# Performance work log

Measured on AMD Instinct MI355X. Metric: run time of the kernel, lower is better.

## Reference

```python
import jax, jax.numpy as jnp
import numpy as np


def setup_inputs() -> dict:
    key = jax.random.key(0)
    ks = jax.random.split(key, 8)
    B, C, H, W = 4, 256, 64, 64
    Cqk = C // 8
    s = 0.05
    return {
        "x": jax.random.normal(ks[0], (B, C, H, W), jnp.float32),
        "Wq": jax.random.normal(ks[1], (Cqk, C), jnp.float32) * s,
        "bq": jax.random.normal(ks[2], (Cqk,), jnp.float32) * s,
        "Wk": jax.random.normal(ks[3], (Cqk, C), jnp.float32) * s,
        "bk": jax.random.normal(ks[4], (Cqk,), jnp.float32) * s,
        "Wv": jax.random.normal(ks[5], (C, C), jnp.float32) * s,
        "bv": jax.random.normal(ks[6], (C,), jnp.float32) * s,
        "gamma": jax.random.normal(ks[7], (1,), jnp.float32),
    }


def reference(x, Wq, bq, Wk, bk, Wv, bv, gamma):
    B, C, H, W = x.shape
    N = H * W
    xf = x.reshape(B, C, N)                      # [B,C,N]
    # 1x1 convs == channel matmuls
    q = jnp.einsum('oc,bcn->bon', Wq, xf) + bq[None, :, None]   # [B,C/8,N]
    k = jnp.einsum('oc,bcn->bon', Wk, xf) + bk[None, :, None]   # [B,C/8,N]
    v = jnp.einsum('oc,bcn->bon', Wv, xf) + bv[None, :, None]   # [B,C,N]
    # scores[b,i,j] = <q[:,i], k[:,j]>; softmax over j (last dim)
    scores = jnp.einsum('bci,bcj->bij', q, k)                   # [B,N,N]
    attn = jax.nn.softmax(scores, axis=-1)
    # out[b,c,i] = sum_j v[b,c,j] * attn[b,i,j]
    out = jnp.einsum('bcj,bij->bci', v, attn).reshape(B, C, H, W)
    return gamma[0] * out + x
```

## Files before the change

kernel.cpp:

```cpp
#include <hip/hip_runtime.h>


#define B_ 4
#define C_ 256
#define N_ 4096
#define CQK 32

typedef __attribute__((ext_vector_type(8))) short short8;
typedef __attribute__((ext_vector_type(4))) short short4v;
typedef __attribute__((ext_vector_type(16))) float f32x16;
typedef __attribute__((ext_vector_type(4))) float f32x4;

__device__ __forceinline__ unsigned short f2bf(float f) {
  unsigned int u = __builtin_bit_cast(unsigned int, f);
  u = (u + 0x7fffu + ((u >> 16) & 1u)) >> 16;
  return (unsigned short)u;
}
__device__ __forceinline__ float bf2f(unsigned short s) {
  unsigned int u = ((unsigned int)s) << 16;
  return __builtin_bit_cast(float, u);
}
__device__ __forceinline__ short f32tof16(float f) {
  const _Float16 hf = (_Float16)f;
  return __builtin_bit_cast(short, hf);
}
__device__ __forceinline__ f32x16 mfma16(short8 a, short8 b, f32x16 c) {
  return __builtin_amdgcn_mfma_f32_32x32x16_bf16(a, b, c, 0, 0, 0);
}
__device__ __forceinline__ int swz64(int row, int col) {
  return row * 64 + ((((col >> 3) ^ row) & 7) << 3) + (col & 7);
}

#define WAITCNT(s) asm volatile("s_waitcnt " s ::: "memory")
#define BARRIER()                         \
  do {                                    \
    __builtin_amdgcn_s_barrier();         \
    asm volatile("" ::: "memory");        \
  } while (0)

__global__ __launch_bounds__(256) void k_prep(
    const float* __restrict__ x, unsigned short* __restrict__ xthi,
    unsigned short* __restrict__ xtlo,
    const float* __restrict__ Wq, const float* __restrict__ Wk,
    const float* __restrict__ Wv,
    unsigned short* __restrict__ wqh, unsigned short* __restrict__ wql,
    unsigned short* __restrict__ wkh, unsigned short* __restrict__ wkl,
    unsigned short* __restrict__ wvh, unsigned short* __restrict__ wvl) {
  __shared__ __align__(16) float tile[64 * 65];
  const int bi = blockIdx.x;
  const int t = threadIdx.x;
  if (bi < 1024) {
    const int it = bi & 63, ct = (bi >> 6) & 3, b = bi >> 8;
    const int i0 = it * 64, c0 = ct * 64;
    {
      const int i = t & 63, cb = t >> 6;
#pragma unroll
      for (int z = 0; z < 16; ++z) {
        const int c = z * 4 + cb;
        tile[i * 65 + c] = x[(b * C_ + c0 + c) * N_ + i0 + i];
      }
    }
    __syncthreads();
    {
      const int ii = t >> 2, p = t & 3;
      short8 h0, h1, l0, l1;
#pragma unroll
      for (int e = 0; e < 16; ++e) {
        const float f = tile[ii * 65 + p * 16 + e];
        const unsigned short hb = f2bf(f);
        const unsigned short lb = f2bf(f - bf2f(hb));
        if (e < 8) { h0[e] = (short)hb; l0[e] = (short)lb; }
        else       { h1[e - 8] = (short)hb; l1[e - 8] = (short)lb; }
      }
      const int base = (b * N_ + i0 + ii) * C_ + c0 + p * 16;
      *(short8*)(xthi + base) = h0;
      *(short8*)(xthi + base + 8) = h1;
      *(short8*)(xtlo + base) = l0;
      *(short8*)(xtlo + base + 8) = l1;
    }
  } else {
    const int e = (bi - 1024) * 256 + t;
    const float* src; unsigned short *hi, *lo; int idx;
    if (e < 8192)        { src = Wq; hi = wqh; lo = wql; idx = e; }
    else if (e < 16384)  { src = Wk; hi = wkh; lo = wkl; idx = e - 8192; }
    else                 { src = Wv; hi = wvh; lo = wvl; idx = e - 16384; }
    const float f = src[idx];
    const unsigned short h = f2bf(f);
    hi[idx] = h;
    lo[idx] = f2bf(f - bf2f(h));
  }
}

__global__ __launch_bounds__(256) void k_proj(
    const unsigned short* __restrict__ wqh, const unsigned short* __restrict__ wql,
    const unsigned short* __restrict__ wkh, const unsigned short* __restrict__ wkl,
    const unsigned short* __restrict__ wvh, const unsigned short* __restrict__ wvl,
    const unsigned short* __restrict__ xthi, const unsigned short* __restrict__ xtlo,
    const float* __restrict__ bq, const float* __restrict__ bk,
    const float* __restrict__ bv,
    unsigned short* __restrict__ qhg, unsigned short* __restrict__ qlg,
    unsigned short* __restrict__ khg, unsigned short* __restrict__ klg,
    unsigned short* __restrict__ vg) {
  __shared__ __align__(16) char sm[33792];
  unsigned short* awh = (unsigned short*)sm;
  unsigned short* awl = awh + 4096;
  unsigned short* bxh = awl + 4096;
  unsigned short* bxl = bxh + 4096;
  float* qt = (float*)sm;

  const int it = blockIdx.x, ot = blockIdx.y, b = blockIdx.z;
  const int i0 = it * 64, o0 = ot * 64;
  const int t = threadIdx.x, lane = t & 63, w = t >> 6, h = lane >> 5;
  const int mb = w >> 1, nb = w & 1;
  const int srow = t >> 2, sp = t & 3;

  const int og = o0 + srow;
  const unsigned short *wh, *wl;
  if (og < 32)      { wh = wqh + og * C_;        wl = wql + og * C_; }
  else if (og < 64) { wh = wkh + (og - 32) * C_; wl = wkl + (og - 32) * C_; }
  else              { wh = wvh + (og - 64) * C_; wl = wvl + (og - 64) * C_; }
  const unsigned short* xh = xthi + (b * N_ + i0 + srow) * C_;
  const unsigned short* xl = xtlo + (b * N_ + i0 + srow) * C_;

  f32x16 acc;
#pragma unroll
  for (int e = 0; e < 16; ++e) acc[e] = 0.f;
  const int m = 32 * mb + (lane & 31);
  const int n = 32 * nb + (lane & 31);

  for (int kt = 0; kt < 4; ++kt) {
    const int cb = kt * 64 + sp * 16;
    *(short8*)&awh[swz64(srow, sp * 16)]     = *(const short8*)(wh + cb);
    *(short8*)&awh[swz64(srow, sp * 16 + 8)] = *(const short8*)(wh + cb + 8);
    *(short8*)&awl[swz64(srow, sp * 16)]     = *(const short8*)(wl + cb);
    *(short8*)&awl[swz64(srow, sp * 16 + 8)] = *(const short8*)(wl + cb + 8);
    *(short8*)&bxh[swz64(srow, sp * 16)]     = *(const short8*)(xh + cb);
    *(short8*)&bxh[swz64(srow, sp * 16 + 8)] = *(const short8*)(xh + cb + 8);
    *(short8*)&bxl[swz64(srow, sp * 16)]     = *(const short8*)(xl + cb);
    *(short8*)&bxl[swz64(srow, sp * 16 + 8)] = *(const short8*)(xl + cb + 8);
    __syncthreads();
#pragma unroll
    for (int kk = 0; kk < 4; ++kk) {
      const int kb = kk * 16 + h * 8;
      const short8 ah  = *(const short8*)&awh[swz64(m, kb)];
      const short8 al2 = *(const short8*)&awl[swz64(m, kb)];
      const short8 bh  = *(const short8*)&bxh[swz64(n, kb)];
      const short8 bl2 = *(const short8*)&bxl[swz64(n, kb)];
      acc = mfma16(ah, bh, acc);
      acc = mfma16(ah, bl2, acc);
      acc = mfma16(al2, bh, acc);
    }
    __syncthreads();
  }

  if (ot > 0) {
#pragma unroll
    for (int e = 0; e < 16; ++e) {
      const int r = 32 * mb + (e & 3) + 8 * (e >> 2) + 4 * h;
      const int oc = o0 - 64 + r;
      vg[(b * C_ + oc) * N_ + i0 + n] = f2bf(acc[e] + bv[oc]);
    }
  } else {
#pragma unroll
    for (int e = 0; e < 16; ++e) {
      const int r = 32 * mb + (e & 3) + 8 * (e >> 2) + 4 * h;
      const float bias = (r < 32) ? bq[r] : bk[r - 32];
      qt[r * 65 + n] = acc[e] + bias;
    }
    __syncthreads();
    const int ii = t >> 2;
    short8 hv0, hv1, lv0, lv1;
#pragma unroll
    for (int e = 0; e < 16; ++e) {
      const float f = qt[(sp * 16 + e) * 65 + ii];
      const unsigned short hb = f2bf(f);
      const unsigned short lb = f2bf(f - bf2f(hb));
      if (e < 8) { hv0[e] = (short)hb; lv0[e] = (short)lb; }
      else       { hv1[e - 8] = (short)hb; lv1[e - 8] = (short)lb; }
    }
    if (sp < 2) {
      const int base = (b * N_ + i0 + ii) * CQK + sp * 16;
      *(short8*)(qhg + base) = hv0; *(short8*)(qhg + base + 8) = hv1;
      *(short8*)(qlg + base) = lv0; *(short8*)(qlg + base + 8) = lv1;
    } else {
      const int base = (b * N_ + i0 + ii) * CQK + sp * 16 - 32;
      *(short8*)(khg + base) = hv0; *(short8*)(khg + base + 8) = hv1;
      *(short8*)(klg + base) = lv0; *(short8*)(klg + base + 8) = lv1;
    }
  }
}

__global__ __launch_bounds__(768, 3) void k_flash(
    const unsigned short* __restrict__ qhg, const unsigned short* __restrict__ qlg,
    const unsigned short* __restrict__ khg, const unsigned short* __restrict__ klg,
    const unsigned short* __restrict__ vg,
    unsigned short* __restrict__ Opart, float* __restrict__ mlpart) {
  __shared__ __align__(16) char sm[17920];
  char* Pb0 = sm;
  char* Pb1 = sm + 8192;
  float* alphaA = (float*)(sm + 16384);
  float* mlm = (float*)(sm + 16896);

  const int blk = blockIdx.x;
  const int b = (blk >> 1) & 3;
  const int half = blk & 1;
  const int qt_ = blk >> 3;
  const int q0 = qt_ * 64;
  const int jbase = half * 2048;
  const int t = threadIdx.x, lane = t & 63, w = t >> 6, h = lane >> 5;
  const int l31 = lane & 31;

  if (w < 8) {
    const int c = 32 * w + l31;
    const unsigned short* vsrc = vg + (size_t)(b * C_ + c) * N_ + jbase + h * 8;
    f32x16 acc0, acc1;
#pragma unroll
    for (int e = 0; e < 16; ++e) { acc0[e] = 0.f; acc1[e] = 0.f; }
    short8 vf[4];
#pragma unroll
    for (int kk = 0; kk < 4; ++kk)
      vf[kk] = *(const short8*)(vsrc + kk * 16);
    WAITCNT("lgkmcnt(0)");
    BARRIER();

#pragma unroll 2
    for (int kt = 0; kt < 32; ++kt) {
      const char* pb = (kt & 1) ? Pb1 : Pb0;
      const float* alp = alphaA + (kt & 1) * 64;
#pragma unroll
      for (int eq = 0; eq < 4; ++eq) {
        const f32x4 av0 = *(const f32x4*)(alp + 8 * eq + 4 * h);
        const f32x4 av1 = *(const f32x4*)(alp + 32 + 8 * eq + 4 * h);
#pragma unroll
        for (int q = 0; q < 4; ++q) {
          acc0[4 * eq + q] *= av0[q];
          acc1[4 * eq + q] *= av1[q];
        }
      }
      __builtin_amdgcn_s_setprio(1);
#pragma unroll
      for (int kk = 0; kk < 4; ++kk) {
        const int phys = (2 * kk + h) ^ (l31 & 7);
        const short8 pa0 = *(const short8*)(pb + l31 * 128 + phys * 16);
        const short8 pa1 = *(const short8*)(pb + (32 + l31) * 128 + phys * 16);
        acc0 = mfma16(pa0, vf[kk], acc0);
        acc1 = mfma16(pa1, vf[kk], acc1);
      }
      __builtin_amdgcn_s_setprio(0);
      if (kt + 1 < 32) {
#pragma unroll
        for (int kk = 0; kk < 4; ++kk)
          vf[kk] = *(const short8*)(vsrc + (kt + 1) * 64 + kk * 16);
      }
      WAITCNT("lgkmcnt(0)");
      BARRIER();
    }
    {
      unsigned short* dst = Opart + (size_t)blk * 16384 + (w * 64 + lane) * 32;
      short8 o0, o1, o2, o3;
#pragma unroll
      for (int e = 0; e < 8; ++e) {
        o0[e] = f32tof16(acc0[e]);
        o1[e] = f32tof16(acc0[8 + e]);
        o2[e] = f32tof16(acc1[e]);
        o3[e] = f32tof16(acc1[8 + e]);
      }
      *(short8*)(dst) = o0;
      *(short8*)(dst + 8) = o1;
      *(short8*)(dst + 16) = o2;
      *(short8*)(dst + 24) = o3;
    }
  } else {
    const int sw = w - 8;
    const int pair = sw >> 1;
    const int rb = sw & 1;
    const int srow = rb * 32 + l31;
    short8 qfh[2], qfl[2];
    {
      const unsigned short* qph = qhg + (size_t)(b * N_ + q0 + srow) * CQK + h * 8;
      const unsigned short* qpl = qlg + (size_t)(b * N_ + q0 + srow) * CQK + h * 8;
#pragma unroll
      for (int kk = 0; kk < 2; ++kk) {
        qfh[kk] = *(const short8*)(qph + kk * 16);
        qfl[kk] = *(const short8*)(qpl + kk * 16);
      }
    }
    const unsigned short* kph = khg + (size_t)(b * N_ + jbase + l31) * CQK + h * 8;
    const unsigned short* kpl = klg + (size_t)(b * N_ + jbase + l31) * CQK + h * 8;
    short8 kfh[2][2], kfl[2][2];
    float m_run = -1e30f, l_run = 0.f;

    auto loadK = [&](int tau) {
#pragma unroll
      for (int jt = 0; jt < 2; ++jt)
#pragma unroll
        for (int kk = 0; kk < 2; ++kk) {
          kfh[jt][kk] = *(const short8*)(kph + tau * 2048 + jt * 1024 + kk * 16);
          kfl[jt][kk] = *(const short8*)(kpl + tau * 2048 + jt * 1024 + kk * 16);
        }
    };
    auto s_step = [&](int tau) {
      f32x16 s0, s1;
#pragma unroll
      for (int e = 0; e < 16; ++e) { s0[e] = 0.f; s1[e] = 0.f; }
      __builtin_amdgcn_s_setprio(1);
#pragma unroll
      for (int kk = 0; kk < 2; ++kk) {
        s0 = mfma16(kfh[0][kk], qfh[kk], s0);
        s0 = mfma16(kfh[0][kk], qfl[kk], s0);
        s0 = mfma16(kfl[0][kk], qfh[kk], s0);
        s1 = mfma16(kfh[1][kk], qfh[kk], s1);
        s1 = mfma16(kfh[1][kk], qfl[kk], s1);
        s1 = mfma16(kfl[1][kk], qfh[kk], s1);
      }
      __builtin_amdgcn_s_setprio(0);
      if (tau + 2 < 32) loadK(tau + 2);
      float mprev, lprev;
      if (tau == 0) { mprev = -1e30f; lprev = 0.f; }
      else {
        mprev = mlm[((tau + 1) & 1) * 128 + srow];
        lprev = mlm[((tau + 1) & 1) * 128 + 64 + srow];
      }
      float mx = s0[0];
#pragma unroll
      for (int e = 1; e < 16; ++e) mx = fmaxf(mx, s0[e]);
#pragma unroll
      for (int e = 0; e < 16; ++e) mx = fmaxf(mx, s1[e]);
      mx = fmaxf(mx, __shfl_xor(mx, 32));
      const float mnew = fmaxf(mprev, mx);
      const float al = __expf(mprev - mnew);
      float ts = 0.f;
#pragma unroll
      for (int e = 0; e < 16; ++e) { s0[e] = __expf(s0[e] - mnew); ts += s0[e]; }
#pragma unroll
      for (int e = 0; e < 16; ++e) { s1[e] = __expf(s1[e] - mnew); ts += s1[e]; }
      ts += __shfl_xor(ts, 32);
      const float lnew = lprev * al + ts;
      m_run = mnew;
      l_run = lnew;
      char* Pw = (tau & 1) ? Pb1 : Pb0;
#pragma unroll
      for (int q = 0; q < 4; ++q) {
        short4v p0, p1;
        p0[0] = (short)f2bf(s0[4 * q]);     p0[1] = (short)f2bf(s0[4 * q + 1]);
        p0[2] = (short)f2bf(s0[4 * q + 2]); p0[3] = (short)f2bf(s0[4 * q + 3]);
        p1[0] = (short)f2bf(s1[4 * q]);     p1[1] = (short)f2bf(s1[4 * q + 1]);
        p1[2] = (short)f2bf(s1[4 * q + 2]); p1[3] = (short)f2bf(s1[4 * q + 3]);
        const int ph0 = q ^ (srow & 7);
        const int ph1 = (4 + q) ^ (srow & 7);
        *(short4v*)(Pw + srow * 128 + ph0 * 16 + 8 * h) = p0;
        *(short4v*)(Pw + srow * 128 + ph1 * 16 + 8 * h) = p1;
      }
      if (h == 0) {
        alphaA[(tau & 1) * 64 + srow] = al;
        mlm[(tau & 1) * 128 + srow] = mnew;
        mlm[(tau & 1) * 128 + 64 + srow] = lnew;
      }
    };

    loadK(pair);
    if (pair == 0) s_step(0);
    WAITCNT("lgkmcnt(0)");
    BARRIER();

#pragma unroll 2
    for (int kt = 0; kt < 32; ++kt) {
      const int tau = kt + 1;
      if (tau < 32 && (tau & 1) == pair) s_step(tau);
      WAITCNT("lgkmcnt(0)");
      BARRIER();
    }
    if (pair == 1 && h == 0) {
      mlpart[blk * 128 + srow] = m_run;
      mlpart[blk * 128 + 64 + srow] = l_run;
    }
  }
}

__global__ __launch_bounds__(256) void k_combine(
    const unsigned short* __restrict__ Opart, const float* __restrict__ mlpart,
    const float* __restrict__ x, const float* __restrict__ gamma,
    float* __restrict__ out) {
  const int cb = blockIdx.x;
  const int b = cb & 3, qt_ = cb >> 2;
  const int q0 = qt_ * 64;
  const int blk1 = (qt_ << 3) | (b << 1);
  const int blk2 = blk1 | 1;
  const int t = threadIdx.x;
  const int i = t & 63, cg = t >> 6;

  const float m1 = mlpart[blk1 * 128 + i], l1 = mlpart[blk1 * 128 + 64 + i];
  const float m2 = mlpart[blk2 * 128 + i], l2 = mlpart[blk2 * 128 + 64 + i];
  const float M = fmaxf(m1, m2);
  const float w1 = __expf(m1 - M), w2 = __expf(m2 - M);
  const float inv = 1.f / (w1 * l1 + w2 * l2);
  const float gm = gamma[0];
  const float s1 = gm * w1 * inv, s2 = gm * w2 * inv;

  const int hh = (i >> 2) & 1;
  const int s = ((i >> 5) << 4) + (((i & 31) >> 3) << 2) + (i & 3);
  const unsigned short* p1 = Opart + (size_t)blk1 * 16384 + hh * 1024 + s;
  const unsigned short* p2 = Opart + (size_t)blk2 * 16384 + hh * 1024 + s;
#pragma unroll 4
  for (int c = cg; c < C_; c += 4) {
    const int lb = (c >> 5) * 2048 + (c & 31) * 32;
    const float o1 = (float)__builtin_bit_cast(_Float16, p1[lb]);
    const float o2 = (float)__builtin_bit_cast(_Float16, p2[lb]);
    const int g = (b * C_ + c) * N_ + q0 + i;
    out[g] = s1 * o1 + s2 * o2 + x[g];
  }
}

extern "C" void kernel_launch(void* const* d_in, const int* in_sizes, int n_in,
                              void* d_out, int out_size, void* d_ws, size_t ws_size,
                              hipStream_t stream) {
  const float* x     = (const float*)d_in[0];
  const float* Wq    = (const float*)d_in[1];
  const float* bq    = (const float*)d_in[2];
  const float* Wk    = (const float*)d_in[3];
  const float* bk    = (const float*)d_in[4];
  const float* Wv    = (const float*)d_in[5];
  const float* bv    = (const float*)d_in[6];
  const float* gamma = (const float*)d_in[7];
  float* out = (float*)d_out;
  (void)in_sizes; (void)n_in; (void)out_size; (void)ws_size;

  char* ws = (char*)d_ws;
  size_t off = 0;
  auto carve = [&](size_t bytes) -> char* {
    char* p = ws + off;
    off += (bytes + 255) & ~(size_t)255;
    return p;
  };
  unsigned short* xthi = (unsigned short*)carve((size_t)B_ * N_ * C_ * 2);
  unsigned short* xtlo = (unsigned short*)carve((size_t)B_ * N_ * C_ * 2);
  unsigned short* wqh  = (unsigned short*)carve(32 * 256 * 2);
  unsigned short* wql  = (unsigned short*)carve(32 * 256 * 2);
  unsigned short* wkh  = (unsigned short*)carve(32 * 256 * 2);
  unsigned short* wkl  = (unsigned short*)carve(32 * 256 * 2);
  unsigned short* wvh  = (unsigned short*)carve(256 * 256 * 2);
  unsigned short* wvl  = (unsigned short*)carve(256 * 256 * 2);
  unsigned short* qhg  = (unsigned short*)carve((size_t)B_ * N_ * CQK * 2);
  unsigned short* qlg  = (unsigned short*)carve((size_t)B_ * N_ * CQK * 2);
  unsigned short* khg  = (unsigned short*)carve((size_t)B_ * N_ * CQK * 2);
  unsigned short* klg  = (unsigned short*)carve((size_t)B_ * N_ * CQK * 2);
  unsigned short* vg   = (unsigned short*)carve((size_t)B_ * C_ * N_ * 2);
  unsigned short* Opart = (unsigned short*)carve((size_t)512 * 16384 * 2);
  float* mlpart = (float*)carve((size_t)512 * 128 * 4);

  k_prep<<<1344, 256, 0, stream>>>(x, xthi, xtlo, Wq, Wk, Wv,
                                   wqh, wql, wkh, wkl, wvh, wvl);
  k_proj<<<dim3(64, 5, B_), 256, 0, stream>>>(wqh, wql, wkh, wkl, wvh, wvl,
                                              xthi, xtlo, bq, bk, bv,
                                              qhg, qlg, khg, klg, vg);
  k_flash<<<512, 768, 0, stream>>>(qhg, qlg, khg, klg, vg, Opart, mlpart);
  k_combine<<<256, 256, 0, stream>>>(Opart, mlpart, x, gamma, out);
}
```

Measured before the change: 188.5 us.

## Restructure flash kernel into fewer wider waves with exp2 softmax and skip-rescale

The flash kernel drops from 12 to 6 waves per block. The 4 PV waves each now compute 64 channels with four accumulators, and the 2 score waves each handle 32 rows on every tile instead of alternating. Q weights and bias are pre-scaled by log2(e) so exp2 replaces exp. A ballot flag lets the PV waves skip rescaling the accumulator when the running max did not change, and P is packed with v_cvt_pk_bf16_f32. The combine indexing follows the new Opart layout. The trade-off is fewer waves to hide latency, more registers per thread, and score computation possibly becoming the critical path.

```diff
diff --git a/kernel.cpp b/kernel.cpp
--- a/kernel.cpp
+++ b/kernel.cpp
@@ -5,9 +5,11 @@
 #define C_ 256
 #define N_ 4096
 #define CQK 32
+#define LOG2E 1.44269504088896340736f
 
 typedef __attribute__((ext_vector_type(8))) short short8;
 typedef __attribute__((ext_vector_type(4))) short short4v;
+typedef __attribute__((ext_vector_type(2))) unsigned int uint2v;
 typedef __attribute__((ext_vector_type(16))) float f32x16;
 typedef __attribute__((ext_vector_type(4))) float f32x4;
 
@@ -23,6 +25,11 @@
 __device__ __forceinline__ short f32tof16(float f) {
   const _Float16 hf = (_Float16)f;
   return __builtin_bit_cast(short, hf);
+}
+__device__ __forceinline__ unsigned int cvtpk(float lo, float hi) {
+  unsigned int r;
+  asm("v_cvt_pk_bf16_f32 %0, %1, %2" : "=v"(r) : "v"(lo), "v"(hi));
+  return r;
 }
 __device__ __forceinline__ f32x16 mfma16(short8 a, short8 b, f32x16 c) {
   return __builtin_amdgcn_mfma_f32_32x32x16_bf16(a, b, c, 0, 0, 0);
@@ -84,7 +91,8 @@
     if (e < 8192)        { src = Wq; hi = wqh; lo = wql; idx = e; }
     else if (e < 16384)  { src = Wk; hi = wkh; lo = wkl; idx = e - 8192; }
     else                 { src = Wv; hi = wvh; lo = wvl; idx = e - 16384; }
-    const float f = src[idx];
+    float f = src[idx];
+    if (e < 8192) f *= LOG2E;
     const unsigned short h = f2bf(f);
     hi[idx] = h;
     lo[idx] = f2bf(f - bf2f(h));
@@ -164,7 +172,7 @@
 #pragma unroll
     for (int e = 0; e < 16; ++e) {
       const int r = 32 * mb + (e & 3) + 8 * (e >> 2) + 4 * h;
-      const float bias = (r < 32) ? bq[r] : bk[r - 32];
+      const float bias = (r < 32) ? bq[r] * LOG2E : bk[r - 32];
       qt[r * 65 + n] = acc[e] + bias;
     }
     __syncthreads();
@@ -190,16 +198,16 @@
   }
 }
 
-__global__ __launch_bounds__(768, 3) void k_flash(
+__global__ __launch_bounds__(384, 3) void k_flash(
     const unsigned short* __restrict__ qhg, const unsigned short* __restrict__ qlg,
     const unsigned short* __restrict__ khg, const unsigned short* __restrict__ klg,
     const unsigned short* __restrict__ vg,
     unsigned short* __restrict__ Opart, float* __restrict__ mlpart) {
-  __shared__ __align__(16) char sm[17920];
+  __shared__ __align__(16) char sm[16928];
   char* Pb0 = sm;
   char* Pb1 = sm + 8192;
   float* alphaA = (float*)(sm + 16384);
-  float* mlm = (float*)(sm + 16896);
+  float* chgF = (float*)(sm + 16896);
 
   const int blk = blockIdx.x;
   const int b = (blk >> 1) & 3;
@@ -210,16 +218,21 @@
   const int t = threadIdx.x, lane = t & 63, w = t >> 6, h = lane >> 5;
   const int l31 = lane & 31;
 
-  if (w < 8) {
-    const int c = 32 * w + l31;
-    const unsigned short* vsrc = vg + (size_t)(b * C_ + c) * N_ + jbase + h * 8;
-    f32x16 acc0, acc1;
-#pragma unroll
-    for (int e = 0; e < 16; ++e) { acc0[e] = 0.f; acc1[e] = 0.f; }
-    short8 vf[4];
-#pragma unroll
-    for (int kk = 0; kk < 4; ++kk)
-      vf[kk] = *(const short8*)(vsrc + kk * 16);
+  if (w < 4) {
+    const int c0 = 64 * w + l31;
+    const unsigned short* vsrc0 = vg + (size_t)(b * C_ + c0) * N_ + jbase + h * 8;
+    const unsigned short* vsrc1 = vsrc0 + (size_t)32 * N_;
+    f32x16 acc0, acc1, acc2, acc3;
+#pragma unroll
+    for (int e = 0; e < 16; ++e) {
+      acc0[e] = 0.f; acc1[e] = 0.f; acc2[e] = 0.f; acc3[e] = 0.f;
+    }
+    short8 vf0[4], vf1[4];
+#pragma unroll
+    for (int kk = 0; kk < 4; ++kk) {
+      vf0[kk] = *(const short8*)(vsrc0 + kk * 16);
+      vf1[kk] = *(const short8*)(vsrc1 + kk * 16);
+    }
     WAITCNT("lgkmcnt(0)");
     BARRIER();
 
@@ -227,14 +240,28 @@
     for (int kt = 0; kt < 32; ++kt) {
       const char* pb = (kt & 1) ? Pb1 : Pb0;
       const float* alp = alphaA + (kt & 1) * 64;
-#pragma unroll
-      for (int eq = 0; eq < 4; ++eq) {
-        const f32x4 av0 = *(const f32x4*)(alp + 8 * eq + 4 * h);
-        const f32x4 av1 = *(const f32x4*)(alp + 32 + 8 * eq + 4 * h);
-#pragma unroll
-        for (int q = 0; q < 4; ++q) {
-          acc0[4 * eq + q] *= av0[q];
-          acc1[4 * eq + q] *= av1[q];
+      const float cA = chgF[(kt & 1) * 2];
+      const float cB = chgF[(kt & 1) * 2 + 1];
+      if (cA != 0.f) {
+#pragma unroll
+        for (int eq = 0; eq < 4; ++eq) {
+          const f32x4 av = *(const f32x4*)(alp + 8 * eq + 4 * h);
+#pragma unroll
+          for (int q = 0; q < 4; ++q) {
+            acc0[4 * eq + q] *= av[q];
+            acc2[4 * eq + q] *= av[q];
+          }
+        }
+      }
+      if (cB != 0.f) {
+#pragma unroll
+        for (int eq = 0; eq < 4; ++eq) {
+          const f32x4 av = *(const f32x4*)(alp + 32 + 8 * eq + 4 * h);
+#pragma unroll
+          for (int q = 0; q < 4; ++q) {
+            acc1[4 * eq + q] *= av[q];
+            acc3[4 * eq + q] *= av[q];
+          }
         }
       }
       __builtin_amdgcn_s_setprio(1);
@@ -243,38 +270,38 @@
         const int phys = (2 * kk + h) ^ (l31 & 7);
         const short8 pa0 = *(const short8*)(pb + l31 * 128 + phys * 16);
         const short8 pa1 = *(const short8*)(pb + (32 + l31) * 128 + phys * 16);
-        acc0 = mfma16(pa0, vf[kk], acc0);
-        acc1 = mfma16(pa1, vf[kk], acc1);
+        acc0 = mfma16(pa0, vf0[kk], acc0);
+        acc1 = mfma16(pa1, vf0[kk], acc1);
+        acc2 = mfma16(pa0, vf1[kk], acc2);
+        acc3 = mfma16(pa1, vf1[kk], acc3);
       }
       __builtin_amdgcn_s_setprio(0);
       if (kt + 1 < 32) {
 #pragma unroll
-        for (int kk = 0; kk < 4; ++kk)
-          vf[kk] = *(const short8*)(vsrc + (kt + 1) * 64 + kk * 16);
+        for (int kk = 0; kk < 4; ++kk) {
+          vf0[kk] = *(const short8*)(vsrc0 + (kt + 1) * 64 + kk * 16);
+          vf1[kk] = *(const short8*)(vsrc1 + (kt + 1) * 64 + kk * 16);
+        }
       }
       WAITCNT("lgkmcnt(0)");
       BARRIER();
     }
     {
-      unsigned short* dst = Opart + (size_t)blk * 16384 + (w * 64 + lane) * 32;
-      short8 o0, o1, o2, o3;
+      unsigned short* dst = Opart + (size_t)blk * 16384 + (w * 64 + lane) * 64;
+      short8 o[8];
 #pragma unroll
       for (int e = 0; e < 8; ++e) {
-        o0[e] = f32tof16(acc0[e]);
-        o1[e] = f32tof16(acc0[8 + e]);
-        o2[e] = f32tof16(acc1[e]);
-        o3[e] = f32tof16(acc1[8 + e]);
-      }
-      *(short8*)(dst) = o0;
-      *(short8*)(dst + 8) = o1;
-      *(short8*)(dst + 16) = o2;
-      *(short8*)(dst + 24) = o3;
+        o[0][e] = f32tof16(acc0[e]);      o[1][e] = f32tof16(acc0[8 + e]);
+        o[2][e] = f32tof16(acc1[e]);      o[3][e] = f32tof16(acc1[8 + e]);
+        o[4][e] = f32tof16(acc2[e]);      o[5][e] = f32tof16(acc2[8 + e]);
+        o[6][e] = f32tof16(acc3[e]);      o[7][e] = f32tof16(acc3[8 + e]);
+      }
+#pragma unroll
+      for (int q = 0; q < 8; ++q) *(short8*)(dst + 8 * q) = o[q];
     }
   } else {
-    const int sw = w - 8;
-    const int pair = sw >> 1;
-    const int rb = sw & 1;
-    const int srow = rb * 32 + l31;
+    const int sw = w - 4;
+    const int srow = sw * 32 + l31;
     short8 qfh[2], qfl[2];
     {
       const unsigned short* qph = qhg + (size_t)(b * N_ + q0 + srow) * CQK + h * 8;
@@ -314,63 +341,65 @@
         s1 = mfma16(kfl[1][kk], qfh[kk], s1);
       }
       __builtin_amdgcn_s_setprio(0);
-      if (tau + 2 < 32) loadK(tau + 2);
-      float mprev, lprev;
-      if (tau == 0) { mprev = -1e30f; lprev = 0.f; }
-      else {
-        mprev = mlm[((tau + 1) & 1) * 128 + srow];
-        lprev = mlm[((tau + 1) & 1) * 128 + 64 + srow];
-      }
-      float mx = s0[0];
-#pragma unroll
-      for (int e = 1; e < 16; ++e) mx = fmaxf(mx, s0[e]);
-#pragma unroll
-      for (int e = 0; e < 16; ++e) mx = fmaxf(mx, s1[e]);
+      if (tau + 1 < 32) loadK(tau + 1);
+      float mx8[8];
+#pragma unroll
+      for (int i2 = 0; i2 < 4; ++i2) {
+        mx8[i2] = fmaxf(fmaxf(s0[4 * i2], s0[4 * i2 + 1]),
+                        fmaxf(s0[4 * i2 + 2], s0[4 * i2 + 3]));
+        mx8[4 + i2] = fmaxf(fmaxf(s1[4 * i2], s1[4 * i2 + 1]),
+                            fmaxf(s1[4 * i2 + 2], s1[4 * i2 + 3]));
+      }
+      float mx = fmaxf(fmaxf(fmaxf(mx8[0], mx8[1]), fmaxf(mx8[2], mx8[3])),
+                       fmaxf(fmaxf(mx8[4], mx8[5]), fmaxf(mx8[6], mx8[7])));
       mx = fmaxf(mx, __shfl_xor(mx, 32));
-      const float mnew = fmaxf(mprev, mx);
-      const float al = __expf(mprev - mnew);
-      float ts = 0.f;
-#pragma unroll
-      for (int e = 0; e < 16; ++e) { s0[e] = __expf(s0[e] - mnew); ts += s0[e]; }
-#pragma unroll
-      for (int e = 0; e < 16; ++e) { s1[e] = __expf(s1[e] - mnew); ts += s1[e]; }
+      const float mnew = fmaxf(m_run, mx);
+      const bool up = mnew > m_run;
+      const float al = __builtin_exp2f(m_run - mnew);
+#pragma unroll
+      for (int e = 0; e < 16; ++e) s0[e] = __builtin_exp2f(s0[e] - mnew);
+#pragma unroll
+      for (int e = 0; e < 16; ++e) s1[e] = __builtin_exp2f(s1[e] - mnew);
+      float t8[8];
+#pragma unroll
+      for (int i2 = 0; i2 < 4; ++i2) {
+        t8[i2] = (s0[4 * i2] + s0[4 * i2 + 1]) + (s0[4 * i2 + 2] + s0[4 * i2 + 3]);
+        t8[4 + i2] = (s1[4 * i2] + s1[4 * i2 + 1]) + (s1[4 * i2 + 2] + s1[4 * i2 + 3]);
+      }
+      float ts = ((t8[0] + t8[1]) + (t8[2] + t8[3])) +
+                 ((t8[4] + t8[5]) + (t8[6] + t8[7]));
       ts += __shfl_xor(ts, 32);
-      const float lnew = lprev * al + ts;
-      m_run = mnew;
-      l_run = lnew;
+      l_run = l_run * al + ts;
       char* Pw = (tau & 1) ? Pb1 : Pb0;
 #pragma unroll
       for (int q = 0; q < 4; ++q) {
-        short4v p0, p1;
-        p0[0] = (short)f2bf(s0[4 * q]);     p0[1] = (short)f2bf(s0[4 * q + 1]);
-        p0[2] = (short)f2bf(s0[4 * q + 2]); p0[3] = (short)f2bf(s0[4 * q + 3]);
-        p1[0] = (short)f2bf(s1[4 * q]);     p1[1] = (short)f2bf(s1[4 * q + 1]);
-        p1[2] = (short)f2bf(s1[4 * q + 2]); p1[3] = (short)f2bf(s1[4 * q + 3]);
+        uint2v u0, u1;
+        u0[0] = cvtpk(s0[4 * q], s0[4 * q + 1]);
+        u0[1] = cvtpk(s0[4 * q + 2], s0[4 * q + 3]);
+        u1[0] = cvtpk(s1[4 * q], s1[4 * q + 1]);
+        u1[1] = cvtpk(s1[4 * q + 2], s1[4 * q + 3]);
         const int ph0 = q ^ (srow & 7);
         const int ph1 = (4 + q) ^ (srow & 7);
-        *(short4v*)(Pw + srow * 128 + ph0 * 16 + 8 * h) = p0;
-        *(short4v*)(Pw + srow * 128 + ph1 * 16 + 8 * h) = p1;
-      }
-      if (h == 0) {
-        alphaA[(tau & 1) * 64 + srow] = al;
-        mlm[(tau & 1) * 128 + srow] = mnew;
-        mlm[(tau & 1) * 128 + 64 + srow] = lnew;
-      }
+        *(uint2v*)(Pw + srow * 128 + ph0 * 16 + 8 * h) = u0;
+        *(uint2v*)(Pw + srow * 128 + ph1 * 16 + 8 * h) = u1;
+      }
+      const unsigned long long ba = __ballot(up);
+      if (h == 0) alphaA[(tau & 1) * 64 + srow] = al;
+      if (lane == 0) chgF[(tau & 1) * 2 + sw] = ba ? 1.f : 0.f;
+      m_run = mnew;
     };
 
-    loadK(pair);
-    if (pair == 0) s_step(0);
+    loadK(0);
+    s_step(0);
     WAITCNT("lgkmcnt(0)");
     BARRIER();
-
 #pragma unroll 2
     for (int kt = 0; kt < 32; ++kt) {
-      const int tau = kt + 1;
-      if (tau < 32 && (tau & 1) == pair) s_step(tau);
+      if (kt + 1 < 32) s_step(kt + 1);
       WAITCNT("lgkmcnt(0)");
       BARRIER();
     }
-    if (pair == 1 && h == 0) {
+    if (h == 0) {
       mlpart[blk * 128 + srow] = m_run;
       mlpart[blk * 128 + 64 + srow] = l_run;
     }
@@ -392,20 +421,22 @@
   const float m1 = mlpart[blk1 * 128 + i], l1 = mlpart[blk1 * 128 + 64 + i];
   const float m2 = mlpart[blk2 * 128 + i], l2 = mlpart[blk2 * 128 + 64 + i];
   const float M = fmaxf(m1, m2);
-  const float w1 = __expf(m1 - M), w2 = __expf(m2 - M);
+  const float w1 = __builtin_exp2f(m1 - M), w2 = __builtin_exp2f(m2 - M);
   const float inv = 1.f / (w1 * l1 + w2 * l2);
   const float gm = gamma[0];
   const float s1 = gm * w1 * inv, s2 = gm * w2 * inv;
 
   const int hh = (i >> 2) & 1;
-  const int s = ((i >> 5) << 4) + (((i & 31) >> 3) << 2) + (i & 3);
-  const unsigned short* p1 = Opart + (size_t)blk1 * 16384 + hh * 1024 + s;
-  const unsigned short* p2 = Opart + (size_t)blk2 * 16384 + hh * 1024 + s;
+  const int e = (i & 3) + 4 * ((i >> 3) & 3);
+  const int rs = i >> 5;
+  const unsigned short* p1 = Opart + (size_t)blk1 * 16384;
+  const unsigned short* p2 = Opart + (size_t)blk2 * 16384;
 #pragma unroll 4
   for (int c = cg; c < C_; c += 4) {
-    const int lb = (c >> 5) * 2048 + (c & 31) * 32;
-    const float o1 = (float)__builtin_bit_cast(_Float16, p1[lb]);
-    const float o2 = (float)__builtin_bit_cast(_Float16, p2[lb]);
+    const int off = (c >> 6) * 4096 + ((c & 31) + 32 * hh) * 64 +
+                    (rs + 2 * ((c >> 5) & 1)) * 16 + e;
+    const float o1 = (float)__builtin_bit_cast(_Float16, p1[off]);
+    const float o2 = (float)__builtin_bit_cast(_Float16, p2[off]);
     const int g = (b * C_ + c) * N_ + q0 + i;
     out[g] = s1 * o1 + s2 * o2 + x[g];
   }
@@ -453,6 +484,6 @@
   k_proj<<<dim3(64, 5, B_), 256, 0, stream>>>(wqh, wql, wkh, wkl, wvh, wvl,
                                               xthi, xtlo, bq, bk, bv,
                                               qhg, qlg, khg, klg, vg);
-  k_flash<<<512, 768, 0, stream>>>(qhg, qlg, khg, klg, vg, Opart, mlpart);
+  k_flash<<<512, 384, 0, stream>>>(qhg, qlg, khg, klg, vg, Opart, mlpart);
   k_combine<<<256, 256, 0, stream>>>(Opart, mlpart, x, gamma, out);
 }
```

After: 187.9 us. About the same (-0.3%).
